# Performance work log

Measured on AMD Instinct MI355X. Metric: run time of the kernel, lower is better.

The kernel has to match this reference:

```python
import jax, jax.numpy as jnp
import numpy as np

NEG_BIG = -9e15  # matches -9000000000000000.0 in the torch source


def setup_inputs() -> dict:
    key = jax.random.key(0)
    k_h, k_adj, k_W, k_a = jax.random.split(key, 4)
    B, N, F_in, F_out = 8, 2048, 256, 256
    h = jax.random.normal(k_h, (B, N, F_in), dtype=jnp.float32)
    adj = jax.random.randint(k_adj, (B, N, N), 0, 2, dtype=jnp.int32)
    # xavier_uniform with gain=1.414
    gain = 1.414
    lim_W = gain * np.sqrt(6.0 / (F_in + F_out))
    W = jax.random.uniform(k_W, (F_in, F_out), dtype=jnp.float32, minval=-lim_W, maxval=lim_W)
    lim_a = gain * np.sqrt(6.0 / (2 * F_out + 1))
    a = jax.random.uniform(k_a, (2 * F_out, 1), dtype=jnp.float32, minval=-lim_a, maxval=lim_a)
    return {"h": h, "adj": adj, "W": W, "a": a}


def reference(h, adj, W, a):
    # h: [B, N, F_in], adj: [B, N, N], W: [F_in, F_out], a: [2*F_out, 1]
    F_out = W.shape[1]
    Wh = jnp.matmul(h, W)  # [B, N, F_out]
    a1 = a[:F_out, 0]      # [F_out]
    a2 = a[F_out:, 0]      # [F_out]
    # e_ij = Wh_i . a1 + Wh_j . a2  (identical to cat([Wh_i, Wh_j]) @ a)
    e = (Wh @ a1)[:, :, None] + (Wh @ a2)[:, None, :]  # [B, N, N]
    # NOTE: the original torch forward applies no LeakyReLU before softmax.
    masked = jnp.where(adj > 0, e, jnp.float32(NEG_BIG))
    attention = jax.nn.softmax(masked, axis=-1)  # [B, N, N]
    # dropout is a no-op in eval mode (training=False)
    h_prime = jnp.matmul(attention, Wh)  # [B, N, F_out]
    return jax.nn.elu(h_prime)
```

## Files before the change

### kernel.cpp

```cpp
#include <hip/hip_runtime.h>
#include <math.h>

using short8   = __attribute__((ext_vector_type(8))) short;
using floatx4  = __attribute__((ext_vector_type(4))) float;
using ushort4v = __attribute__((ext_vector_type(4))) unsigned short;
using uint4v   = __attribute__((ext_vector_type(4))) unsigned int;

__device__ __forceinline__ unsigned short f2bf(float x) {
  union { float f; unsigned u; } v; v.f = x;
  unsigned r = (v.u + 0x7FFFu + ((v.u >> 16) & 1u)) >> 16;
  return (unsigned short)r;
}
__device__ __forceinline__ float bf2f(unsigned short u) {
  union { unsigned u; float f; } v; v.u = ((unsigned)u) << 16;
  return v.f;
}
__device__ __forceinline__ short8 cvt8(const float* p) {
  float4 v0 = *(const float4*)p;
  float4 v1 = *(const float4*)(p + 4);
  short8 r;
  r[0] = (short)f2bf(v0.x); r[1] = (short)f2bf(v0.y);
  r[2] = (short)f2bf(v0.z); r[3] = (short)f2bf(v0.w);
  r[4] = (short)f2bf(v1.x); r[5] = (short)f2bf(v1.y);
  r[6] = (short)f2bf(v1.z); r[7] = (short)f2bf(v1.w);
  return r;
}
__device__ __forceinline__ short8 bc8(uint4v v) {
  union { uint4v u; short8 s; } x; x.u = v; return x.s;
}

__global__ __launch_bounds__(256) void adj_pack(
    const int* __restrict__ adj, unsigned* __restrict__ pk) {
  size_t tid = (size_t)blockIdx.x * 256 + threadIdx.x;
  const int* src = adj + tid * 32;
  unsigned r = 0;
#pragma unroll
  for (int q = 0; q < 8; ++q) {
    int4 v = *(const int4*)(src + q * 4);
    r |= ((unsigned)v.x << (4 * q)) | ((unsigned)v.y << (4 * q + 1)) |
         ((unsigned)v.z << (4 * q + 2)) | ((unsigned)v.w << (4 * q + 3));
  }
  pk[tid] = r;
}

__global__ __launch_bounds__(256) void wt_conv(
    const float* __restrict__ W, unsigned short* __restrict__ Wt) {
  int c = blockIdx.x;
  int k = threadIdx.x;
  int kt = k >> 5, kc = (k >> 3) & 3, e = k & 7;
  size_t dst = (size_t)kt * 16384 + (size_t)(c >> 4) * 1024
             + (size_t)(kc * 16 + (c & 15)) * 16 + e * 2;
  *(unsigned short*)((char*)Wt + dst) = f2bf(W[(size_t)k * 256 + c]);
}

__global__ __launch_bounds__(256) void wh_mfma(
    const float* __restrict__ h, const unsigned short* __restrict__ Wt,
    unsigned short* __restrict__ Whb, const float* __restrict__ a,
    float* __restrict__ g) {
  const int m0 = blockIdx.x * 32;
  const int t  = threadIdx.x;
  const int w  = t >> 6, L = t & 63;
  const int fr = L & 15, kc = L >> 4;

  const float* hrow0 = h + (size_t)(m0 + fr) * 256;
  const float* hrow1 = h + (size_t)(m0 + 16 + fr) * 256;
  const char*  WtB   = (const char*)Wt;

  floatx4 acc[2][4];
#pragma unroll
  for (int i = 0; i < 2; ++i)
#pragma unroll
    for (int n = 0; n < 4; ++n) acc[i][n] = (floatx4)0.0f;

#pragma unroll
  for (int kt = 0; kt < 8; ++kt) {
    short8 a0 = cvt8(hrow0 + kt * 32 + kc * 8);
    short8 a1 = cvt8(hrow1 + kt * 32 + kc * 8);
#pragma unroll
    for (int nf = 0; nf < 4; ++nf) {
      short8 bf = *(const short8*)(WtB + (size_t)kt * 16384
                                   + (size_t)(w * 4 + nf) * 1024 + (size_t)L * 16);
      acc[0][nf] = __builtin_amdgcn_mfma_f32_16x16x32_bf16(a0, bf, acc[0][nf], 0, 0, 0);
      acc[1][nf] = __builtin_amdgcn_mfma_f32_16x16x32_bf16(a1, bf, acc[1][nf], 0, 0, 0);
    }
  }

  const int q = L >> 4;
  float a2v[4];
#pragma unroll
  for (int nf = 0; nf < 4; ++nf) a2v[nf] = a[256 + w * 64 + nf * 16 + fr];
#pragma unroll
  for (int mf = 0; mf < 2; ++mf) {
    float p[4] = {0.f, 0.f, 0.f, 0.f};
#pragma unroll
    for (int nf = 0; nf < 4; ++nf) {
#pragma unroll
      for (int jj = 0; jj < 4; ++jj) {
        int row = m0 + mf * 16 + q * 4 + jj;
        Whb[(size_t)row * 256 + w * 64 + nf * 16 + fr] = f2bf(acc[mf][nf][jj]);
        p[jj] += acc[mf][nf][jj] * a2v[nf];
      }
    }
#pragma unroll
    for (int jj = 0; jj < 4; ++jj) {
#pragma unroll
      for (int off = 1; off < 16; off <<= 1) p[jj] += __shfl_xor(p[jj], off);
      if (fr == 0) atomicAdd(&g[m0 + mf * 16 + q * 4 + jj], p[jj]);
    }
  }
}

__global__ __launch_bounds__(256) void batch_max(
    const float* __restrict__ g, float* __restrict__ Mb) {
  __shared__ float red[4];
  int b = blockIdx.x, t = threadIdx.x;
  float m = -1e30f;
  for (int i = t; i < 2048; i += 256) m = fmaxf(m, g[(size_t)b * 2048 + i]);
#pragma unroll
  for (int off = 32; off > 0; off >>= 1) m = fmaxf(m, __shfl_xor(m, off));
  if ((t & 63) == 0) red[t >> 6] = m;
  __syncthreads();
  if (t == 0) Mb[b] = fmaxf(fmaxf(red[0], red[1]), fmaxf(red[2], red[3]));
}

__global__ __launch_bounds__(256) void build_bt(
    const unsigned short* __restrict__ Whb, const float* __restrict__ g,
    const float* __restrict__ Mb, unsigned short* __restrict__ Bt) {
  __shared__ __align__(16) unsigned short tile[320 * 72];
  const int blk = blockIdx.x;
  const int b   = blk >> 5;
  const int j0  = (blk & 31) * 64;
  const int kt_base = (blk & 31) * 2;
  const int t   = threadIdx.x;
  const int j   = t & 63;
  const int q0  = t >> 6;
  const int row = b * 2048 + j0 + j;
  const float s = expf(g[row] - Mb[b]);
  for (int q = q0; q < 64; q += 4) {
    ushort4v wv = *(const ushort4v*)&Whb[(size_t)row * 256 + q * 4];
    int c = q * 4;
    tile[(c + 0) * 72 + j] = f2bf(s * bf2f(wv[0]));
    tile[(c + 1) * 72 + j] = f2bf(s * bf2f(wv[1]));
    tile[(c + 2) * 72 + j] = f2bf(s * bf2f(wv[2]));
    tile[(c + 3) * 72 + j] = f2bf(s * bf2f(wv[3]));
  }
  if (q0 == 0) tile[256 * 72 + j] = f2bf(s);
  for (int z = t; z < 63 * 64; z += 256) {
    int c = 257 + (z >> 6);
    tile[c * 72 + (z & 63)] = 0;
  }
  __syncthreads();
#pragma unroll
  for (int p = 0; p < 10; ++p) {
    int id   = t + 256 * p;
    int fr   = id & 15;
    int slot = (id >> 4) & 3;
    int rest = id >> 6;
    int nfg  = rest % 20;
    int kt_l = rest / 20;
    const unsigned short* src = &tile[(nfg * 16 + fr) * 72 + kt_l * 32 + slot * 8];
    size_t dst = (size_t)(b * 64 + kt_base + kt_l) * 20480
               + (size_t)nfg * 1024 + (size_t)(slot * 16 + fr) * 16;
    *(int4*)((char*)Bt + dst) = *(const int4*)src;
  }
}

__global__ __launch_bounds__(512, 1) void gat_main(
    const unsigned* __restrict__ pk, const unsigned short* __restrict__ Bt,
    float* __restrict__ out) {
  __shared__ __align__(16) char lds[64 * 272 + 256];
  const int bid = blockIdx.x;
  const int b   = bid & 7;
  const int rb  = bid >> 3;
  const int i0  = rb * 64;
  const int tid = threadIdx.x;
  const int w   = tid >> 6, L = tid & 63;
  const int wm  = w >> 2, wn = w & 3;
  const int fr  = L & 15, kc = L >> 4;

  {
    int r = tid >> 3, seg = tid & 7;
    const char* src = (const char*)pk + ((size_t)(b * 2048 + i0 + r) * 256 + seg * 32);
    char* dst = lds + r * 272 + seg * 32;
    *(int4*)(dst)      = *(const int4*)(src);
    *(int4*)(dst + 16) = *(const int4*)(src + 16);
  }
  __syncthreads();

  const char* bsrc = (const char*)Bt + (size_t)b * 1310720
                   + (size_t)(wn * 5) * 1024 + (size_t)L * 16;
  const char* arow0 = lds + (wm * 32 + fr) * 272;
  const char* arow1 = arow0 + 16 * 272;
  const int   ksh   = kc * 8;

  floatx4 acc[2][5];
#pragma unroll
  for (int i = 0; i < 2; ++i)
#pragma unroll
    for (int n = 0; n < 5; ++n) acc[i][n] = (floatx4)0.0f;

  uint4v s0_0, s0_1, s0_2, s0_3, s0_4;
  uint4v s1_0, s1_1, s1_2, s1_3, s1_4;
  uint4v s2_0, s2_1, s2_2, s2_3, s2_4;

#define GL(DST, P, OFF) \
  asm volatile("global_load_dwordx4 %0, %1, off offset:" #OFF \
               : "=v"(DST) : "v"(P))

#define LOADB(TT, SET) {                                  \
    const char* p_ = bsrc + (size_t)(TT) * 20480;         \
    const char* q_ = p_ + 4096;                           \
    GL(SET##_0, p_, 0);                                   \
    GL(SET##_1, p_, 1024);                                \
    GL(SET##_2, p_, 2048);                                \
    GL(SET##_3, p_, 3072);                                \
    GL(SET##_4, q_, 0);                                   \
  }

#define GATE(N) {                                         \
    asm volatile("s_waitcnt vmcnt(" #N ")");              \
    __builtin_amdgcn_sched_barrier(0);                    \
  }

#define AFRAG(WORD, DST) {                                \
    unsigned x_ = ((WORD) >> ksh) & 0xFFu;                \
    unsigned y_ = x_ | (x_ << 15);                        \
    union { unsigned u[4]; short8 s; } c_;                \
    c_.u[0] = (y_        & 0x10001u) * 0x3F80u;           \
    c_.u[1] = ((y_ >> 2) & 0x10001u) * 0x3F80u;           \
    c_.u[2] = ((y_ >> 4) & 0x10001u) * 0x3F80u;           \
    c_.u[3] = ((y_ >> 6) & 0x10001u) * 0x3F80u;           \
    DST = c_.s;                                           \
  }

#define COMPUTE(TT, SET) {                                                       \
    unsigned aw0_ = *(const unsigned*)(arow0 + (TT) * 4);                        \
    unsigned aw1_ = *(const unsigned*)(arow1 + (TT) * 4);                        \
    short8 af0_, af1_;                                                           \
    AFRAG(aw0_, af0_);                                                           \
    AFRAG(aw1_, af1_);                                                           \
    short8 b0_ = bc8(SET##_0), b1_ = bc8(SET##_1), b2_ = bc8(SET##_2);           \
    short8 b3_ = bc8(SET##_3), b4_ = bc8(SET##_4);                               \
    acc[0][0] = __builtin_amdgcn_mfma_f32_16x16x32_bf16(af0_, b0_, acc[0][0], 0, 0, 0); \
    acc[1][0] = __builtin_amdgcn_mfma_f32_16x16x32_bf16(af1_, b0_, acc[1][0], 0, 0, 0); \
    acc[0][1] = __builtin_amdgcn_mfma_f32_16x16x32_bf16(af0_, b1_, acc[0][1], 0, 0, 0); \
    acc[1][1] = __builtin_amdgcn_mfma_f32_16x16x32_bf16(af1_, b1_, acc[1][1], 0, 0, 0); \
    acc[0][2] = __builtin_amdgcn_mfma_f32_16x16x32_bf16(af0_, b2_, acc[0][2], 0, 0, 0); \
    acc[1][2] = __builtin_amdgcn_mfma_f32_16x16x32_bf16(af1_, b2_, acc[1][2], 0, 0, 0); \
    acc[0][3] = __builtin_amdgcn_mfma_f32_16x16x32_bf16(af0_, b3_, acc[0][3], 0, 0, 0); \
    acc[1][3] = __builtin_amdgcn_mfma_f32_16x16x32_bf16(af1_, b3_, acc[1][3], 0, 0, 0); \
    acc[0][4] = __builtin_amdgcn_mfma_f32_16x16x32_bf16(af0_, b4_, acc[0][4], 0, 0, 0); \
    acc[1][4] = __builtin_amdgcn_mfma_f32_16x16x32_bf16(af1_, b4_, acc[1][4], 0, 0, 0); \
  }

  LOADB(0, s0); LOADB(1, s1); LOADB(2, s2);

#pragma unroll 1
  for (int kt = 0; kt < 60; kt += 3) {
    GATE(10); COMPUTE(kt + 0, s0); LOADB(kt + 3, s0);
    GATE(10); COMPUTE(kt + 1, s1); LOADB(kt + 4, s1);
    GATE(10); COMPUTE(kt + 2, s2); LOADB(kt + 5, s2);
  }
  GATE(10); COMPUTE(60, s0); LOADB(63, s0);
  GATE(10); COMPUTE(61, s1);
  GATE(5);  COMPUTE(62, s2);
  GATE(0);  COMPUTE(63, s0);

  float* denL = (float*)(lds + 64 * 272);
  const int q = L >> 4;
  if (wn == 3 && fr == 0) {
#pragma unroll
    for (int mf = 0; mf < 2; ++mf)
#pragma unroll
      for (int jj = 0; jj < 4; ++jj)
        denL[wm * 32 + mf * 16 + q * 4 + jj] = acc[mf][1][jj];
  }
  __syncthreads();
  float invd[2][4];
#pragma unroll
  for (int mf = 0; mf < 2; ++mf)
#pragma unroll
    for (int jj = 0; jj < 4; ++jj)
      invd[mf][jj] = 1.0f / denL[wm * 32 + mf * 16 + q * 4 + jj];
#pragma unroll
  for (int mf = 0; mf < 2; ++mf) {
#pragma unroll
    for (int nf = 0; nf < 5; ++nf) {
      int col = wn * 80 + nf * 16 + fr;
      if (col < 256) {
#pragma unroll
        for (int jj = 0; jj < 4; ++jj) {
          int row = wm * 32 + mf * 16 + q * 4 + jj;
          float v = acc[mf][nf][jj] * invd[mf][jj];
          v = (v > 0.0f) ? v : expm1f(v);
          out[((size_t)b * 2048 + i0 + row) * 256 + col] = v;
        }
      }
    }
  }
#undef COMPUTE
#undef AFRAG
#undef GATE
#undef LOADB
#undef GL
}

extern "C" void kernel_launch(void* const* d_in, const int* in_sizes, int n_in,
                              void* d_out, int out_size, void* d_ws, size_t ws_size,
                              hipStream_t stream) {
  const float* h   = (const float*)d_in[0];
  const int*   adj = (const int*)d_in[1];
  const float* W   = (const float*)d_in[2];
  const float* a   = (const float*)d_in[3];
  float* out = (float*)d_out;

  char* ws = (char*)d_ws;
  if (ws_size < 23265536) return;
  unsigned short* Whb = (unsigned short*)ws;
  float* g            = (float*)(ws + 8388608);
  float* Mb           = (float*)(ws + 8454144);
  unsigned short* Bt  = (unsigned short*)(ws + 8454400);
  unsigned short* Wt  = (unsigned short*)(ws + 18940160);
  unsigned* pk        = (unsigned*)(ws + 19071232);

  hipMemsetAsync(g, 0, 65536, stream);
  adj_pack <<<4096, 256, 0, stream>>>(adj, pk);
  wt_conv  <<<256,  256, 0, stream>>>(W, Wt);
  wh_mfma  <<<512,  256, 0, stream>>>(h, Wt, Whb, a, g);
  batch_max<<<8,    256, 0, stream>>>(g, Mb);
  build_bt <<<256,  256, 0, stream>>>(Whb, g, Mb, Bt);
  gat_main <<<256,  512, 0, stream>>>(pk, Bt, out);
}
```

Baseline: 88.05 us.

## Fuse adjacency bit-packing into main kernel with pipelined adj loads

Removes the separate adj_pack kernel and its packed-mask buffer. The main GAT kernel now streams raw int32 adjacency rows in segments of 256 columns, packs them to bits with wave shuffles into LDS, and overlaps those loads with the MFMA/B-tile pipeline. This avoids a kernel launch and a round-trip write and read of the packed mask. In exchange it adds extra vmcnt bookkeeping, a barrier per segment, and more registers in the main loop.

```diff
diff --git a/kernel.cpp b/kernel.cpp
--- a/kernel.cpp
+++ b/kernel.cpp
@@ -27,20 +27,6 @@
 }
 __device__ __forceinline__ short8 bc8(uint4v v) {
   union { uint4v u; short8 s; } x; x.u = v; return x.s;
-}
-
-__global__ __launch_bounds__(256) void adj_pack(
-    const int* __restrict__ adj, unsigned* __restrict__ pk) {
-  size_t tid = (size_t)blockIdx.x * 256 + threadIdx.x;
-  const int* src = adj + tid * 32;
-  unsigned r = 0;
-#pragma unroll
-  for (int q = 0; q < 8; ++q) {
-    int4 v = *(const int4*)(src + q * 4);
-    r |= ((unsigned)v.x << (4 * q)) | ((unsigned)v.y << (4 * q + 1)) |
-         ((unsigned)v.z << (4 * q + 2)) | ((unsigned)v.w << (4 * q + 3));
-  }
-  pk[tid] = r;
 }
 
 __global__ __launch_bounds__(256) void wt_conv(
@@ -166,7 +152,7 @@
 }
 
 __global__ __launch_bounds__(512, 1) void gat_main(
-    const unsigned* __restrict__ pk, const unsigned short* __restrict__ Bt,
+    const int* __restrict__ adj, const unsigned short* __restrict__ Bt,
     float* __restrict__ out) {
   __shared__ __align__(16) char lds[64 * 272 + 256];
   const int bid = blockIdx.x;
@@ -178,15 +164,7 @@
   const int wm  = w >> 2, wn = w & 3;
   const int fr  = L & 15, kc = L >> 4;
 
-  {
-    int r = tid >> 3, seg = tid & 7;
-    const char* src = (const char*)pk + ((size_t)(b * 2048 + i0 + r) * 256 + seg * 32);
-    char* dst = lds + r * 272 + seg * 32;
-    *(int4*)(dst)      = *(const int4*)(src);
-    *(int4*)(dst + 16) = *(const int4*)(src + 16);
-  }
-  __syncthreads();
-
+  const char* adjB = (const char*)adj + ((size_t)b * 2048 + i0) * 8192;
   const char* bsrc = (const char*)Bt + (size_t)b * 1310720
                    + (size_t)(wn * 5) * 1024 + (size_t)L * 16;
   const char* arow0 = lds + (wm * 32 + fr) * 272;
@@ -202,6 +180,7 @@
   uint4v s0_0, s0_1, s0_2, s0_3, s0_4;
   uint4v s1_0, s1_1, s1_2, s1_3, s1_4;
   uint4v s2_0, s2_1, s2_2, s2_3, s2_4;
+  uint4v aj[8];
 
 #define GL(DST, P, OFF) \
   asm volatile("global_load_dwordx4 %0, %1, off offset:" #OFF \
@@ -217,9 +196,33 @@
     GL(SET##_4, q_, 0);                                   \
   }
 
-#define GATE(N) {                                         \
+#define GATE_(N) {                                        \
     asm volatile("s_waitcnt vmcnt(" #N ")");              \
     __builtin_amdgcn_sched_barrier(0);                    \
+  }
+#define GATE(N) GATE_(N)
+
+#define ADJLOADS(SEG) {                                   \
+    const char* ap_ = adjB + (size_t)(SEG) * 1024 + (size_t)L * 16; \
+    _Pragma("unroll")                                     \
+    for (int ri = 0; ri < 8; ++ri)                        \
+      GL(aj[ri], ap_ + (size_t)(w * 8 + ri) * 8192, 0);   \
+  }
+
+#define PACK(SEG) {                                                   \
+    _Pragma("unroll")                                                 \
+    for (int ri = 0; ri < 8; ++ri) {                                  \
+      unsigned nb = aj[ri][0] | (aj[ri][1] << 1)                      \
+                  | (aj[ri][2] << 2) | (aj[ri][3] << 3);              \
+      unsigned o_ = __shfl_xor(nb, 1);                                \
+      nb = (L & 1) ? (o_ | (nb << 4)) : (nb | (o_ << 4));             \
+      o_ = __shfl_xor(nb, 2);                                         \
+      nb = (L & 2) ? (o_ | (nb << 8)) : (nb | (o_ << 8));             \
+      o_ = __shfl_xor(nb, 4);                                         \
+      nb = (L & 4) ? (o_ | (nb << 16)) : (nb | (o_ << 16));           \
+      if ((L & 7) == 0)                                               \
+        *(unsigned*)(lds + (w * 8 + ri) * 272 + (SEG) * 32 + (L >> 3) * 4) = nb; \
+    }                                                                 \
   }
 
 #define AFRAG(WORD, DST) {                                \
@@ -253,18 +256,39 @@
     acc[1][4] = __builtin_amdgcn_mfma_f32_16x16x32_bf16(af1_, b4_, acc[1][4], 0, 0, 0); \
   }
 
-  LOADB(0, s0); LOADB(1, s1); LOADB(2, s2);
+  ADJLOADS(0);
+  asm volatile("s_waitcnt vmcnt(0)");
+  __builtin_amdgcn_sched_barrier(0);
+  PACK(0);
+  __syncthreads();
 
 #pragma unroll 1
-  for (int kt = 0; kt < 60; kt += 3) {
-    GATE(10); COMPUTE(kt + 0, s0); LOADB(kt + 3, s0);
-    GATE(10); COMPUTE(kt + 1, s1); LOADB(kt + 4, s1);
-    GATE(10); COMPUTE(kt + 2, s2); LOADB(kt + 5, s2);
-  }
-  GATE(10); COMPUTE(60, s0); LOADB(63, s0);
-  GATE(10); COMPUTE(61, s1);
-  GATE(5);  COMPUTE(62, s2);
-  GATE(0);  COMPUTE(63, s0);
+  for (int s = 0; s < 7; ++s) {
+    int T = s * 8;
+    LOADB(T + 0, s0); LOADB(T + 1, s1); LOADB(T + 2, s2);
+    ADJLOADS(s + 1);
+    GATE(18); COMPUTE(T + 0, s0); LOADB(T + 3, s0);
+    GATE(13); COMPUTE(T + 1, s1); LOADB(T + 4, s1);
+    GATE(13); COMPUTE(T + 2, s2); LOADB(T + 5, s2);
+    GATE(10); COMPUTE(T + 3, s0); LOADB(T + 6, s0);
+    GATE(10); COMPUTE(T + 4, s1); LOADB(T + 7, s1);
+    GATE(10); COMPUTE(T + 5, s2);
+    GATE(5);  COMPUTE(T + 6, s0);
+    GATE(0);  COMPUTE(T + 7, s1);
+    PACK(s + 1);
+    __syncthreads();
+  }
+  {
+    LOADB(56, s0); LOADB(57, s1); LOADB(58, s2);
+    GATE(10); COMPUTE(56, s0); LOADB(59, s0);
+    GATE(10); COMPUTE(57, s1); LOADB(60, s1);
+    GATE(10); COMPUTE(58, s2); LOADB(61, s2);
+    GATE(10); COMPUTE(59, s0); LOADB(62, s0);
+    GATE(10); COMPUTE(60, s1); LOADB(63, s1);
+    GATE(10); COMPUTE(61, s2);
+    GATE(5);  COMPUTE(62, s0);
+    GATE(0);  COMPUTE(63, s1);
+  }
 
   float* denL = (float*)(lds + 64 * 272);
   const int q = L >> 4;
@@ -300,7 +324,10 @@
   }
 #undef COMPUTE
 #undef AFRAG
+#undef PACK
+#undef ADJLOADS
 #undef GATE
+#undef GATE_
 #undef LOADB
 #undef GL
 }
@@ -315,19 +342,17 @@
   float* out = (float*)d_out;
 
   char* ws = (char*)d_ws;
-  if (ws_size < 23265536) return;
+  if (ws_size < 19071232) return;
   unsigned short* Whb = (unsigned short*)ws;
   float* g            = (float*)(ws + 8388608);
   float* Mb           = (float*)(ws + 8454144);
   unsigned short* Bt  = (unsigned short*)(ws + 8454400);
   unsigned short* Wt  = (unsigned short*)(ws + 18940160);
-  unsigned* pk        = (unsigned*)(ws + 19071232);
 
   hipMemsetAsync(g, 0, 65536, stream);
-  adj_pack <<<4096, 256, 0, stream>>>(adj, pk);
-  wt_conv  <<<256,  256, 0, stream>>>(W, Wt);
-  wh_mfma  <<<512,  256, 0, stream>>>(h, Wt, Whb, a, g);
-  batch_max<<<8,    256, 0, stream>>>(g, Mb);
-  build_bt <<<256,  256, 0, stream>>>(Whb, g, Mb, Bt);
-  gat_main <<<256,  512, 0, stream>>>(pk, Bt, out);
-}
+  wt_conv  <<<256, 256, 0, stream>>>(W, Wt);
+  wh_mfma  <<<512, 256, 0, stream>>>(h, Wt, Whb, a, g);
+  batch_max<<<8,   256, 0, stream>>>(g, Mb);
+  build_bt <<<256, 256, 0, stream>>>(Whb, g, Mb, Bt);
+  gat_main <<<256, 512, 0, stream>>>(adj, Bt, out);
+}
```

New measurement: 91.79 us. 1.04x slower.

## Split K dimension across two wave groups in gat_main with LDS reduction

Applied to the files above, without the earlier changes.

Doubles gat_main's block from 512 to 1024 threads. The two halves of 8 waves each process half of the 64 K-tiles, and the upper half's partial accumulators are added into the lower half's through LDS before normalisation and ELU. This aims to raise in-flight memory and MFMA parallelism per CU, since the grid is only 256 blocks, one per CU. In exchange it adds a large LDS reduction buffer, extra barriers, and an epilogue that only half the threads run.

```diff
diff --git a/kernel.cpp b/kernel.cpp
--- a/kernel.cpp
+++ b/kernel.cpp
@@ -165,25 +165,25 @@
   }
 }
 
-__global__ __launch_bounds__(512, 1) void gat_main(
+__global__ __launch_bounds__(1024, 1) void gat_main(
     const unsigned* __restrict__ pk, const unsigned short* __restrict__ Bt,
     float* __restrict__ out) {
-  __shared__ __align__(16) char lds[64 * 272 + 256];
+  __shared__ __align__(16) char lds[84224];
   const int bid = blockIdx.x;
   const int b   = bid & 7;
   const int rb  = bid >> 3;
   const int i0  = rb * 64;
   const int tid = threadIdx.x;
   const int w   = tid >> 6, L = tid & 63;
-  const int wm  = w >> 2, wn = w & 3;
+  const int kh  = w >> 3;
+  const int wm  = (w >> 2) & 1, wn = w & 3;
   const int fr  = L & 15, kc = L >> 4;
+  const int t0  = kh * 32;
 
   {
-    int r = tid >> 3, seg = tid & 7;
-    const char* src = (const char*)pk + ((size_t)(b * 2048 + i0 + r) * 256 + seg * 32);
-    char* dst = lds + r * 272 + seg * 32;
-    *(int4*)(dst)      = *(const int4*)(src);
-    *(int4*)(dst + 16) = *(const int4*)(src + 16);
+    int r = tid >> 4, seg = tid & 15;
+    const char* src = (const char*)pk + ((size_t)(b * 2048 + i0 + r) * 256 + seg * 16);
+    *(int4*)(lds + r * 272 + seg * 16) = *(const int4*)(src);
   }
   __syncthreads();
 
@@ -253,22 +253,47 @@
     acc[1][4] = __builtin_amdgcn_mfma_f32_16x16x32_bf16(af1_, b4_, acc[1][4], 0, 0, 0); \
   }
 
-  LOADB(0, s0); LOADB(1, s1); LOADB(2, s2);
+  LOADB(t0 + 0, s0); LOADB(t0 + 1, s1); LOADB(t0 + 2, s2);
 
 #pragma unroll 1
-  for (int kt = 0; kt < 60; kt += 3) {
-    GATE(10); COMPUTE(kt + 0, s0); LOADB(kt + 3, s0);
-    GATE(10); COMPUTE(kt + 1, s1); LOADB(kt + 4, s1);
-    GATE(10); COMPUTE(kt + 2, s2); LOADB(kt + 5, s2);
-  }
-  GATE(10); COMPUTE(60, s0); LOADB(63, s0);
-  GATE(10); COMPUTE(61, s1);
-  GATE(5);  COMPUTE(62, s2);
-  GATE(0);  COMPUTE(63, s0);
-
-  float* denL = (float*)(lds + 64 * 272);
+  for (int kt = 0; kt < 27; kt += 3) {
+    int T = t0 + kt;
+    GATE(10); COMPUTE(T + 0, s0); LOADB(T + 3, s0);
+    GATE(10); COMPUTE(T + 1, s1); LOADB(T + 4, s1);
+    GATE(10); COMPUTE(T + 2, s2); LOADB(T + 5, s2);
+  }
+  GATE(10); COMPUTE(t0 + 27, s0); LOADB(t0 + 30, s0);
+  GATE(10); COMPUTE(t0 + 28, s1); LOADB(t0 + 31, s1);
+  GATE(10); COMPUTE(t0 + 29, s2);
+  GATE(5);  COMPUTE(t0 + 30, s0);
+  GATE(0);  COMPUTE(t0 + 31, s1);
+
+  float* xbuf = (float*)lds;
+  const int slot = ((wm * 4 + wn) * 64 + L) * 41;
+  __syncthreads();
+  if (kh == 1) {
+#pragma unroll
+    for (int i = 0; i < 2; ++i)
+#pragma unroll
+      for (int n = 0; n < 5; ++n)
+#pragma unroll
+        for (int j = 0; j < 4; ++j)
+          xbuf[slot + (i * 5 + n) * 4 + j] = acc[i][n][j];
+  }
+  __syncthreads();
+  if (kh == 0) {
+#pragma unroll
+    for (int i = 0; i < 2; ++i)
+#pragma unroll
+      for (int n = 0; n < 5; ++n)
+#pragma unroll
+        for (int j = 0; j < 4; ++j)
+          acc[i][n][j] += xbuf[slot + (i * 5 + n) * 4 + j];
+  }
+
+  float* denL = (float*)(lds + 83968);
   const int q = L >> 4;
-  if (wn == 3 && fr == 0) {
+  if (kh == 0 && wn == 3 && fr == 0) {
 #pragma unroll
     for (int mf = 0; mf < 2; ++mf)
 #pragma unroll
@@ -276,24 +301,26 @@
         denL[wm * 32 + mf * 16 + q * 4 + jj] = acc[mf][1][jj];
   }
   __syncthreads();
-  float invd[2][4];
-#pragma unroll
-  for (int mf = 0; mf < 2; ++mf)
-#pragma unroll
-    for (int jj = 0; jj < 4; ++jj)
-      invd[mf][jj] = 1.0f / denL[wm * 32 + mf * 16 + q * 4 + jj];
-#pragma unroll
-  for (int mf = 0; mf < 2; ++mf) {
-#pragma unroll
-    for (int nf = 0; nf < 5; ++nf) {
-      int col = wn * 80 + nf * 16 + fr;
-      if (col < 256) {
-#pragma unroll
-        for (int jj = 0; jj < 4; ++jj) {
-          int row = wm * 32 + mf * 16 + q * 4 + jj;
-          float v = acc[mf][nf][jj] * invd[mf][jj];
-          v = (v > 0.0f) ? v : expm1f(v);
-          out[((size_t)b * 2048 + i0 + row) * 256 + col] = v;
+  if (kh == 0) {
+    float invd[2][4];
+#pragma unroll
+    for (int mf = 0; mf < 2; ++mf)
+#pragma unroll
+      for (int jj = 0; jj < 4; ++jj)
+        invd[mf][jj] = 1.0f / denL[wm * 32 + mf * 16 + q * 4 + jj];
+#pragma unroll
+    for (int mf = 0; mf < 2; ++mf) {
+#pragma unroll
+      for (int nf = 0; nf < 5; ++nf) {
+        int col = wn * 80 + nf * 16 + fr;
+        if (col < 256) {
+#pragma unroll
+          for (int jj = 0; jj < 4; ++jj) {
+            int row = wm * 32 + mf * 16 + q * 4 + jj;
+            float v = acc[mf][nf][jj] * invd[mf][jj];
+            v = (v > 0.0f) ? v : expm1f(v);
+            out[((size_t)b * 2048 + i0 + row) * 256 + col] = v;
+          }
         }
       }
     }
@@ -329,5 +356,5 @@
   wh_mfma  <<<512,  256, 0, stream>>>(h, Wt, Whb, a, g);
   batch_max<<<8,    256, 0, stream>>>(g, Mb);
   build_bt <<<256,  256, 0, stream>>>(Whb, g, Mb, Bt);
-  gat_main <<<256,  512, 0, stream>>>(pk, Bt, out);
-}
+  gat_main <<<256, 1024, 0, stream>>>(pk, Bt, out);
+}
```

After: 88.29 us. No clear change (+0.3%).

## Use 4 waves per block with each wave covering all 64 rows

Applied to the files above, without the earlier changes.

Changes gat_main from 8 waves (2x4 split over rows and columns) to 4 waves, each computing all 64 rows for its 80-column slice. Each B-tile global load now feeds four row fragments instead of two, halving the redundant B traffic per block. The cost is half as many waves per CU for hiding latency, double the accumulator registers per thread (80 floats), and fewer waves issuing MFMAs.

```diff
diff --git a/kernel.cpp b/kernel.cpp
--- a/kernel.cpp
+++ b/kernel.cpp
@@ -165,7 +165,7 @@
   }
 }
 
-__global__ __launch_bounds__(512, 1) void gat_main(
+__global__ __launch_bounds__(256, 1) void gat_main(
     const unsigned* __restrict__ pk, const unsigned short* __restrict__ Bt,
     float* __restrict__ out) {
   __shared__ __align__(16) char lds[64 * 272 + 256];
@@ -175,27 +175,30 @@
   const int i0  = rb * 64;
   const int tid = threadIdx.x;
   const int w   = tid >> 6, L = tid & 63;
-  const int wm  = w >> 2, wn = w & 3;
   const int fr  = L & 15, kc = L >> 4;
 
   {
-    int r = tid >> 3, seg = tid & 7;
-    const char* src = (const char*)pk + ((size_t)(b * 2048 + i0 + r) * 256 + seg * 32);
-    char* dst = lds + r * 272 + seg * 32;
+    int r = tid >> 2, seg = tid & 3;
+    const char* src = (const char*)pk + ((size_t)(b * 2048 + i0 + r) * 256 + seg * 64);
+    char* dst = lds + r * 272 + seg * 64;
     *(int4*)(dst)      = *(const int4*)(src);
     *(int4*)(dst + 16) = *(const int4*)(src + 16);
+    *(int4*)(dst + 32) = *(const int4*)(src + 32);
+    *(int4*)(dst + 48) = *(const int4*)(src + 48);
   }
   __syncthreads();
 
   const char* bsrc = (const char*)Bt + (size_t)b * 1310720
-                   + (size_t)(wn * 5) * 1024 + (size_t)L * 16;
-  const char* arow0 = lds + (wm * 32 + fr) * 272;
+                   + (size_t)(w * 5) * 1024 + (size_t)L * 16;
+  const char* arow0 = lds + fr * 272;
   const char* arow1 = arow0 + 16 * 272;
+  const char* arow2 = arow0 + 32 * 272;
+  const char* arow3 = arow0 + 48 * 272;
   const int   ksh   = kc * 8;
 
-  floatx4 acc[2][5];
-#pragma unroll
-  for (int i = 0; i < 2; ++i)
+  floatx4 acc[4][5];
+#pragma unroll
+  for (int i = 0; i < 4; ++i)
 #pragma unroll
     for (int n = 0; n < 5; ++n) acc[i][n] = (floatx4)0.0f;
 
@@ -234,23 +237,34 @@
   }
 
 #define COMPUTE(TT, SET) {                                                       \
-    unsigned aw0_ = *(const unsigned*)(arow0 + (TT) * 4);                        \
-    unsigned aw1_ = *(const unsigned*)(arow1 + (TT) * 4);                        \
-    short8 af0_, af1_;                                                           \
-    AFRAG(aw0_, af0_);                                                           \
-    AFRAG(aw1_, af1_);                                                           \
+    unsigned w0_ = *(const unsigned*)(arow0 + (TT) * 4);                         \
+    unsigned w1_ = *(const unsigned*)(arow1 + (TT) * 4);                         \
+    unsigned w2_ = *(const unsigned*)(arow2 + (TT) * 4);                         \
+    unsigned w3_ = *(const unsigned*)(arow3 + (TT) * 4);                         \
+    short8 af0_, af1_, af2_, af3_;                                               \
+    AFRAG(w0_, af0_); AFRAG(w1_, af1_); AFRAG(w2_, af2_); AFRAG(w3_, af3_);      \
     short8 b0_ = bc8(SET##_0), b1_ = bc8(SET##_1), b2_ = bc8(SET##_2);           \
     short8 b3_ = bc8(SET##_3), b4_ = bc8(SET##_4);                               \
     acc[0][0] = __builtin_amdgcn_mfma_f32_16x16x32_bf16(af0_, b0_, acc[0][0], 0, 0, 0); \
     acc[1][0] = __builtin_amdgcn_mfma_f32_16x16x32_bf16(af1_, b0_, acc[1][0], 0, 0, 0); \
+    acc[2][0] = __builtin_amdgcn_mfma_f32_16x16x32_bf16(af2_, b0_, acc[2][0], 0, 0, 0); \
+    acc[3][0] = __builtin_amdgcn_mfma_f32_16x16x32_bf16(af3_, b0_, acc[3][0], 0, 0, 0); \
     acc[0][1] = __builtin_amdgcn_mfma_f32_16x16x32_bf16(af0_, b1_, acc[0][1], 0, 0, 0); \
     acc[1][1] = __builtin_amdgcn_mfma_f32_16x16x32_bf16(af1_, b1_, acc[1][1], 0, 0, 0); \
+    acc[2][1] = __builtin_amdgcn_mfma_f32_16x16x32_bf16(af2_, b1_, acc[2][1], 0, 0, 0); \
+    acc[3][1] = __builtin_amdgcn_mfma_f32_16x16x32_bf16(af3_, b1_, acc[3][1], 0, 0, 0); \
     acc[0][2] = __builtin_amdgcn_mfma_f32_16x16x32_bf16(af0_, b2_, acc[0][2], 0, 0, 0); \
     acc[1][2] = __builtin_amdgcn_mfma_f32_16x16x32_bf16(af1_, b2_, acc[1][2], 0, 0, 0); \
+    acc[2][2] = __builtin_amdgcn_mfma_f32_16x16x32_bf16(af2_, b2_, acc[2][2], 0, 0, 0); \
+    acc[3][2] = __builtin_amdgcn_mfma_f32_16x16x32_bf16(af3_, b2_, acc[3][2], 0, 0, 0); \
     acc[0][3] = __builtin_amdgcn_mfma_f32_16x16x32_bf16(af0_, b3_, acc[0][3], 0, 0, 0); \
     acc[1][3] = __builtin_amdgcn_mfma_f32_16x16x32_bf16(af1_, b3_, acc[1][3], 0, 0, 0); \
+    acc[2][3] = __builtin_amdgcn_mfma_f32_16x16x32_bf16(af2_, b3_, acc[2][3], 0, 0, 0); \
+    acc[3][3] = __builtin_amdgcn_mfma_f32_16x16x32_bf16(af3_, b3_, acc[3][3], 0, 0, 0); \
     acc[0][4] = __builtin_amdgcn_mfma_f32_16x16x32_bf16(af0_, b4_, acc[0][4], 0, 0, 0); \
     acc[1][4] = __builtin_amdgcn_mfma_f32_16x16x32_bf16(af1_, b4_, acc[1][4], 0, 0, 0); \
+    acc[2][4] = __builtin_amdgcn_mfma_f32_16x16x32_bf16(af2_, b4_, acc[2][4], 0, 0, 0); \
+    acc[3][4] = __builtin_amdgcn_mfma_f32_16x16x32_bf16(af3_, b4_, acc[3][4], 0, 0, 0); \
   }
 
   LOADB(0, s0); LOADB(1, s1); LOADB(2, s2);
@@ -268,29 +282,29 @@
 
   float* denL = (float*)(lds + 64 * 272);
   const int q = L >> 4;
-  if (wn == 3 && fr == 0) {
-#pragma unroll
-    for (int mf = 0; mf < 2; ++mf)
+  if (w == 3 && fr == 0) {
+#pragma unroll
+    for (int mf = 0; mf < 4; ++mf)
 #pragma unroll
       for (int jj = 0; jj < 4; ++jj)
-        denL[wm * 32 + mf * 16 + q * 4 + jj] = acc[mf][1][jj];
+        denL[mf * 16 + q * 4 + jj] = acc[mf][1][jj];
   }
   __syncthreads();
-  float invd[2][4];
-#pragma unroll
-  for (int mf = 0; mf < 2; ++mf)
+  float invd[4][4];
+#pragma unroll
+  for (int mf = 0; mf < 4; ++mf)
 #pragma unroll
     for (int jj = 0; jj < 4; ++jj)
-      invd[mf][jj] = 1.0f / denL[wm * 32 + mf * 16 + q * 4 + jj];
-#pragma unroll
-  for (int mf = 0; mf < 2; ++mf) {
+      invd[mf][jj] = 1.0f / denL[mf * 16 + q * 4 + jj];
+#pragma unroll
+  for (int mf = 0; mf < 4; ++mf) {
 #pragma unroll
     for (int nf = 0; nf < 5; ++nf) {
-      int col = wn * 80 + nf * 16 + fr;
+      int col = w * 80 + nf * 16 + fr;
       if (col < 256) {
 #pragma unroll
         for (int jj = 0; jj < 4; ++jj) {
-          int row = wm * 32 + mf * 16 + q * 4 + jj;
+          int row = mf * 16 + q * 4 + jj;
           float v = acc[mf][nf][jj] * invd[mf][jj];
           v = (v > 0.0f) ? v : expm1f(v);
           out[((size_t)b * 2048 + i0 + row) * 256 + col] = v;
@@ -329,5 +343,5 @@
   wh_mfma  <<<512,  256, 0, stream>>>(h, Wt, Whb, a, g);
   batch_max<<<8,    256, 0, stream>>>(g, Mb);
   build_bt <<<256,  256, 0, stream>>>(Whb, g, Mb, Bt);
-  gat_main <<<256,  512, 0, stream>>>(pk, Bt, out);
-}
+  gat_main <<<256,  256, 0, stream>>>(pk, Bt, out);
+}
```

New measurement: 88.84 us. No clear change (+0.9%).
